# Optimization experiments

Measured on AMD Instinct MI355X. Metric: run time of the kernel, lower is better.

Reference implementation:

```python
import jax, jax.numpy as jnp
import numpy as np

H = 1024      # hidden_size
V = 32000     # output_size (vocab)
L = 128       # max_length (encoder length)
B = 256       # batch


def setup_inputs() -> dict:
    key = jax.random.key(0)
    ks = jax.random.split(key, 16)
    s = 1.0 / np.sqrt(H)
    inp = {
        "input_ids": jax.random.randint(ks[0], (1, B), 0, V),
        "hidden": jax.random.normal(ks[1], (1, B, H), dtype=jnp.float32),
        "encoder_outputs": jax.random.normal(ks[2], (B, L, H), dtype=jnp.float32),
        # parameters
        "emb_table": jax.random.normal(ks[3], (V, H), dtype=jnp.float32),
        "attn_w": jax.random.uniform(ks[4], (L, 2 * H), jnp.float32, -s, s),
        "attn_b": jax.random.uniform(ks[5], (L,), jnp.float32, -s, s),
        "comb_w": jax.random.uniform(ks[6], (H, 2 * H), jnp.float32, -s, s),
        "comb_b": jax.random.uniform(ks[7], (H,), jnp.float32, -s, s),
        "w_ih": jax.random.uniform(ks[8], (3 * H, H), jnp.float32, -s, s),
        "b_ih": jax.random.uniform(ks[9], (3 * H,), jnp.float32, -s, s),
        "w_hh": jax.random.uniform(ks[10], (3 * H, H), jnp.float32, -s, s),
        "b_hh": jax.random.uniform(ks[11], (3 * H,), jnp.float32, -s, s),
        "out_w": jax.random.uniform(ks[12], (V, H), jnp.float32, -s, s),
        "out_b": jax.random.uniform(ks[13], (V,), jnp.float32, -s, s),
    }
    return inp


def reference(input_ids, hidden, encoder_outputs, emb_table,
              attn_w, attn_b, comb_w, comb_b,
              w_ih, b_ih, w_hh, b_hh, out_w, out_b):
    # embedding: input_ids (1, B) -> embedded (1, B, H); dropout is identity in eval
    embedded = emb_table[input_ids]            # (1, B, H)
    emb0 = embedded[0]                         # (B, H)
    h0 = hidden[0]                             # (B, H)

    # Bahdanau-style attention over fixed encoder length L
    attn_logits = jnp.concatenate([emb0, h0], axis=1) @ attn_w.T + attn_b   # (B, L)
    attn_weights = jax.nn.softmax(attn_logits, axis=1)                      # (B, L)
    attn_applied = jnp.einsum("bl,blh->bh", attn_weights, encoder_outputs)  # (B, H)

    # combine + relu
    x = jnp.concatenate([emb0, attn_applied], axis=1) @ comb_w.T + comb_b   # (B, H)
    x = jax.nn.relu(x)

    # single GRU step (PyTorch gate layout: r, z, n)
    gx = x @ w_ih.T + b_ih                     # (B, 3H)
    gh = h0 @ w_hh.T + b_hh                    # (B, 3H)
    xr, xz, xn = jnp.split(gx, 3, axis=1)
    hr, hz, hn = jnp.split(gh, 3, axis=1)
    r = jax.nn.sigmoid(xr + hr)
    z = jax.nn.sigmoid(xz + hz)
    n = jnp.tanh(xn + r * hn)
    h_new = (1.0 - z) * n + z * h0             # (B, H)

    logp = jax.nn.log_softmax(h_new @ out_w.T + out_b, axis=1)   # (B, V)
    return logp, h_new[None], attn_weights
```

## Files before the change

kernel.cpp:

```cpp
#include <hip/hip_runtime.h>
#include <hip/hip_bf16.h>
#include <math.h>

#define H 1024
#define L 128
#define B 256
#define V 32000

typedef __attribute__((ext_vector_type(8))) short bf16x8;
typedef __attribute__((ext_vector_type(4))) float f32x4;

static __device__ __forceinline__ ushort f2bf(float f) {
    unsigned int u = __float_as_uint(f);
    u += 0x7fffu + ((u >> 16) & 1u);
    return (ushort)(u >> 16);
}

__global__ __launch_bounds__(256) void attn_kernel(
    const int* __restrict__ input_ids,
    const float* __restrict__ hidden,
    const float* __restrict__ enc,
    const float* __restrict__ emb_table,
    const float* __restrict__ attn_w,
    const float* __restrict__ attn_b,
    ushort* __restrict__ xcat_b16,
    ushort* __restrict__ h0_b16,
    float* __restrict__ attn_weights_out)
{
    __shared__ float s_e[H];
    __shared__ float s_h[H];
    __shared__ float s_part[256];
    __shared__ float s_w[L];
    __shared__ float s_wr[4];

    const int b = blockIdx.x;
    const int tid = threadIdx.x;

    const int id = input_ids[b];
    const float4* e4 = (const float4*)(emb_table + (size_t)id * H);
    const float4* h4 = (const float4*)(hidden + (size_t)b * H);

    float4 ev = e4[tid];
    float4 hv = h4[tid];
    ((float4*)s_e)[tid] = ev;
    ((float4*)s_h)[tid] = hv;

    {
        uint2 p;
        p.x = (unsigned)f2bf(ev.x) | ((unsigned)f2bf(ev.y) << 16);
        p.y = (unsigned)f2bf(ev.z) | ((unsigned)f2bf(ev.w) << 16);
        *(uint2*)(xcat_b16 + (size_t)b * 2 * H + tid * 4) = p;
        uint2 q;
        q.x = (unsigned)f2bf(hv.x) | ((unsigned)f2bf(hv.y) << 16);
        q.y = (unsigned)f2bf(hv.z) | ((unsigned)f2bf(hv.w) << 16);
        *(uint2*)(h0_b16 + (size_t)b * H + tid * 4) = q;
    }
    __syncthreads();

    const int l = tid & 127;
    const int half = tid >> 7;
    const float4* w4 = (const float4*)(attn_w + (size_t)l * (2 * H) + half * H);
    const float4* s4 = (const float4*)(half ? s_h : s_e);
    float acc = 0.f;
#pragma unroll 4
    for (int k = 0; k < H / 4; ++k) {
        float4 w = w4[k];
        float4 s = s4[k];
        acc += w.x * s.x + w.y * s.y + w.z * s.z + w.w * s.w;
    }
    s_part[tid] = acc;
    __syncthreads();
    if (tid < L) s_w[tid] = s_part[tid] + s_part[tid + 128] + attn_b[tid];
    __syncthreads();

    const int wid = tid >> 6;
    float v = (tid < L) ? s_w[tid] : -INFINITY;
    for (int off = 32; off; off >>= 1) v = fmaxf(v, __shfl_xor(v, off));
    if ((tid & 63) == 0) s_wr[wid] = v;
    __syncthreads();
    const float m = fmaxf(s_wr[0], s_wr[1]);

    float e = 0.f;
    if (tid < L) e = __expf(s_w[tid] - m);
    float sv = e;
    for (int off = 32; off; off >>= 1) sv += __shfl_xor(sv, off);
    __syncthreads();
    if ((tid & 63) == 0) s_wr[wid] = sv;
    __syncthreads();
    const float inv = 1.f / (s_wr[0] + s_wr[1]);
    if (tid < L) {
        float w = e * inv;
        s_w[tid] = w;
        attn_weights_out[(size_t)b * L + tid] = w;
    }
    __syncthreads();

    const float4* enc4 = (const float4*)(enc + (size_t)b * L * H);
    float4 a = {0.f, 0.f, 0.f, 0.f};
#pragma unroll 4
    for (int ll = 0; ll < L; ++ll) {
        const float w = s_w[ll];
        float4 e2 = enc4[(size_t)ll * (H / 4) + tid];
        a.x += w * e2.x; a.y += w * e2.y; a.z += w * e2.z; a.w += w * e2.w;
    }
    {
        uint2 p;
        p.x = (unsigned)f2bf(a.x) | ((unsigned)f2bf(a.y) << 16);
        p.y = (unsigned)f2bf(a.z) | ((unsigned)f2bf(a.w) << 16);
        *(uint2*)(xcat_b16 + (size_t)b * 2 * H + H + tid * 4) = p;
    }
}

template<int K, int MODE>
__global__ __launch_bounds__(256) void mfma_gemm(
    const ushort* __restrict__ A,
    const float* __restrict__ W,
    const float* __restrict__ bias,
    float* __restrict__ outf,
    ushort* __restrict__ outb,
    float* __restrict__ rowsum,
    int N)
{
    constexpr int NT = 32;
    __shared__ ushort sA[256 * 72];
    __shared__ ushort sW[NT * 72];
    __shared__ float sLse[256];

    const int tid = threadIdx.x;
    const int bn = blockIdx.x * NT;
    const int w = tid >> 6;
    const int l = tid & 63;
    const int g = l >> 4;
    const int ln = l & 15;
    const int trow = tid >> 3;
    const int tcol = tid & 7;

    if (MODE == 3) sLse[tid] = __logf(rowsum[tid]);

    f32x4 acc[4][2];
#pragma unroll
    for (int i = 0; i < 4; ++i)
#pragma unroll
        for (int n = 0; n < 2; ++n)
            acc[i][n] = (f32x4){0.f, 0.f, 0.f, 0.f};

    for (int k0 = 0; k0 < K; k0 += 64) {
#pragma unroll
        for (int p = 0; p < 8; ++p) {
            const int r = p * 32 + trow;
            uint4 v = *(const uint4*)(A + (size_t)r * K + k0 + tcol * 8);
            *(uint4*)(sA + r * 72 + tcol * 8) = v;
        }
        {
            const float* wp = W + (size_t)(bn + trow) * K + k0 + tcol * 8;
            float4 w0 = *(const float4*)(wp);
            float4 w1 = *(const float4*)(wp + 4);
            ushort tmp[8];
            tmp[0] = f2bf(w0.x); tmp[1] = f2bf(w0.y); tmp[2] = f2bf(w0.z); tmp[3] = f2bf(w0.w);
            tmp[4] = f2bf(w1.x); tmp[5] = f2bf(w1.y); tmp[6] = f2bf(w1.z); tmp[7] = f2bf(w1.w);
            *(uint4*)(sW + trow * 72 + tcol * 8) = *(const uint4*)tmp;
        }
        __syncthreads();
#pragma unroll
        for (int s = 0; s < 2; ++s) {
            bf16x8 af[4], bfr[2];
#pragma unroll
            for (int i = 0; i < 4; ++i)
                af[i] = *(const bf16x8*)(sA + (64 * w + 16 * i + ln) * 72 + s * 32 + g * 8);
#pragma unroll
            for (int n = 0; n < 2; ++n)
                bfr[n] = *(const bf16x8*)(sW + (16 * n + ln) * 72 + s * 32 + g * 8);
#pragma unroll
            for (int i = 0; i < 4; ++i)
#pragma unroll
                for (int n = 0; n < 2; ++n)
                    acc[i][n] = __builtin_amdgcn_mfma_f32_16x16x32_bf16(af[i], bfr[n], acc[i][n], 0, 0, 0);
        }
        __syncthreads();
    }

    const float b0 = bias[bn + ln];
    const float b1 = bias[bn + 16 + ln];

    if (MODE == 0) {
#pragma unroll
        for (int i = 0; i < 4; ++i)
#pragma unroll
            for (int n = 0; n < 2; ++n)
#pragma unroll
                for (int r = 0; r < 4; ++r)
                    outf[(size_t)(64 * w + 16 * i + 4 * g + r) * N + bn + 16 * n + ln] =
                        acc[i][n][r] + (n ? b1 : b0);
    } else if (MODE == 1) {
#pragma unroll
        for (int i = 0; i < 4; ++i)
#pragma unroll
            for (int n = 0; n < 2; ++n)
#pragma unroll
                for (int r = 0; r < 4; ++r) {
                    float vv = acc[i][n][r] + (n ? b1 : b0);
                    vv = fmaxf(vv, 0.f);
                    outb[(size_t)(64 * w + 16 * i + 4 * g + r) * N + bn + 16 * n + ln] = f2bf(vv);
                }
    } else if (MODE == 2) {
#pragma unroll
        for (int i = 0; i < 4; ++i) {
            float e[4];
#pragma unroll
            for (int r = 0; r < 4; ++r)
                e[r] = __expf(acc[i][0][r] + b0) + __expf(acc[i][1][r] + b1);
#pragma unroll
            for (int msk = 1; msk < 16; msk <<= 1)
#pragma unroll
                for (int r = 0; r < 4; ++r)
                    e[r] += __shfl_xor(e[r], msk);
            if (ln < 4)
                atomicAdd(&rowsum[64 * w + 16 * i + 4 * g + ln], e[ln]);
        }
    } else {
#pragma unroll
        for (int i = 0; i < 4; ++i)
#pragma unroll
            for (int n = 0; n < 2; ++n)
#pragma unroll
                for (int r = 0; r < 4; ++r) {
                    const int row = 64 * w + 16 * i + 4 * g + r;
                    outf[(size_t)row * N + bn + 16 * n + ln] =
                        acc[i][n][r] + (n ? b1 : b0) - sLse[row];
                }
    }
}

__global__ __launch_bounds__(256) void gru_kernel(
    const float* __restrict__ gx,
    const float* __restrict__ gh,
    const float* __restrict__ h0,
    float* __restrict__ h_new,
    ushort* __restrict__ hn_b16,
    float* __restrict__ rowsum)
{
    if (blockIdx.x == 0) rowsum[threadIdx.x] = 0.f;
    const int idx = blockIdx.x * 256 + threadIdx.x;
    const int b = idx >> 10;
    const int j = idx & (H - 1);
    const size_t base = (size_t)b * 3 * H;
    const float xr = gx[base + j];
    const float xz = gx[base + H + j];
    const float xn = gx[base + 2 * H + j];
    const float hr = gh[base + j];
    const float hz = gh[base + H + j];
    const float hn = gh[base + 2 * H + j];
    const float r = 1.f / (1.f + __expf(-(xr + hr)));
    const float z = 1.f / (1.f + __expf(-(xz + hz)));
    const float n = tanhf(xn + r * hn);
    const float out = (1.f - z) * n + z * h0[idx];
    h_new[idx] = out;
    hn_b16[idx] = f2bf(out);
}

extern "C" void kernel_launch(void* const* d_in, const int* in_sizes, int n_in,
                              void* d_out, int out_size, void* d_ws, size_t ws_size,
                              hipStream_t stream) {
    const int*   input_ids = (const int*)d_in[0];
    const float* hidden    = (const float*)d_in[1];
    const float* enc       = (const float*)d_in[2];
    const float* emb_table = (const float*)d_in[3];
    const float* attn_w    = (const float*)d_in[4];
    const float* attn_b    = (const float*)d_in[5];
    const float* comb_w    = (const float*)d_in[6];
    const float* comb_b    = (const float*)d_in[7];
    const float* w_ih      = (const float*)d_in[8];
    const float* b_ih      = (const float*)d_in[9];
    const float* w_hh      = (const float*)d_in[10];
    const float* b_hh      = (const float*)d_in[11];
    const float* out_w     = (const float*)d_in[12];
    const float* out_b     = (const float*)d_in[13];

    float* out = (float*)d_out;
    float* logp         = out;
    float* h_new        = out + (size_t)B * V;
    float* attn_weights = h_new + (size_t)B * H;

    ushort* xcat_b16 = (ushort*)d_ws;
    ushort* h0_b16   = xcat_b16 + (size_t)B * 2 * H;
    ushort* x_b16    = h0_b16 + (size_t)B * H;
    ushort* hn_b16   = x_b16 + (size_t)B * H;
    float*  gx       = (float*)(hn_b16 + (size_t)B * H);
    float*  gh       = gx + (size_t)B * 3 * H;
    float*  rowsum   = gh + (size_t)B * 3 * H;

    attn_kernel<<<dim3(B), dim3(256), 0, stream>>>(
        input_ids, hidden, enc, emb_table, attn_w, attn_b,
        xcat_b16, h0_b16, attn_weights);

    mfma_gemm<2 * H, 1><<<dim3(H / 32), dim3(256), 0, stream>>>(
        xcat_b16, comb_w, comb_b, nullptr, x_b16, nullptr, H);

    mfma_gemm<H, 0><<<dim3(3 * H / 32), dim3(256), 0, stream>>>(
        x_b16, w_ih, b_ih, gx, nullptr, nullptr, 3 * H);

    mfma_gemm<H, 0><<<dim3(3 * H / 32), dim3(256), 0, stream>>>(
        h0_b16, w_hh, b_hh, gh, nullptr, nullptr, 3 * H);

    gru_kernel<<<dim3(B * H / 256), dim3(256), 0, stream>>>(
        gx, gh, hidden, h_new, hn_b16, rowsum);

    mfma_gemm<H, 2><<<dim3(V / 32), dim3(256), 0, stream>>>(
        hn_b16, out_w, out_b, nullptr, nullptr, rowsum, V);

    mfma_gemm<H, 3><<<dim3(V / 32), dim3(256), 0, stream>>>(
        hn_b16, out_w, out_b, logp, nullptr, rowsum, V);
}
```

Before: 589.2 us.

## Split attention apply across blocks, add M-tiling and register prefetch to GEMMs

Attention is split in two kernels. One computes the softmax weights. The other applies them to the encoder outputs over an (8, B) grid, so each batch row's 512KB read is spread across more blocks. The generic GEMM gains template parameters for block size and M/N tile sizes plus a 2D grid, so the small GEMMs launch many more blocks. It also prefetches the next K-slice into registers while MFMA runs on the current one. The vocab GEMMs now use 512-thread blocks with 64-wide N tiles, which halves W re-reads per block but raises register pressure.

```diff
diff --git a/kernel.cpp b/kernel.cpp
--- a/kernel.cpp
+++ b/kernel.cpp
@@ -16,10 +16,9 @@
     return (ushort)(u >> 16);
 }
 
-__global__ __launch_bounds__(256) void attn_kernel(
+__global__ __launch_bounds__(256) void attn_softmax_kernel(
     const int* __restrict__ input_ids,
     const float* __restrict__ hidden,
-    const float* __restrict__ enc,
     const float* __restrict__ emb_table,
     const float* __restrict__ attn_w,
     const float* __restrict__ attn_b,
@@ -37,11 +36,8 @@
     const int tid = threadIdx.x;
 
     const int id = input_ids[b];
-    const float4* e4 = (const float4*)(emb_table + (size_t)id * H);
-    const float4* h4 = (const float4*)(hidden + (size_t)b * H);
-
-    float4 ev = e4[tid];
-    float4 hv = h4[tid];
+    float4 ev = ((const float4*)(emb_table + (size_t)id * H))[tid];
+    float4 hv = ((const float4*)(hidden + (size_t)b * H))[tid];
     ((float4*)s_e)[tid] = ev;
     ((float4*)s_h)[tid] = hv;
 
@@ -88,31 +84,53 @@
     if ((tid & 63) == 0) s_wr[wid] = sv;
     __syncthreads();
     const float inv = 1.f / (s_wr[0] + s_wr[1]);
-    if (tid < L) {
-        float w = e * inv;
-        s_w[tid] = w;
-        attn_weights_out[(size_t)b * L + tid] = w;
-    }
-    __syncthreads();
-
-    const float4* enc4 = (const float4*)(enc + (size_t)b * L * H);
+    if (tid < L) attn_weights_out[(size_t)b * L + tid] = e * inv;
+}
+
+__global__ __launch_bounds__(256) void attn_apply_kernel(
+    const float* __restrict__ enc,
+    const float* __restrict__ attn_weights,
+    ushort* __restrict__ xcat_b16)
+{
+    __shared__ float s_w[L];
+    __shared__ float4 s_red[256];
+
+    const int c = blockIdx.x;
+    const int b = blockIdx.y;
+    const int tid = threadIdx.x;
+    const int lg = tid >> 5;
+    const int hc = tid & 31;
+
+    if (tid < L) s_w[tid] = attn_weights[(size_t)b * L + tid];
+    __syncthreads();
+
+    const float4* enc4 = (const float4*)enc;
     float4 a = {0.f, 0.f, 0.f, 0.f};
-#pragma unroll 4
-    for (int ll = 0; ll < L; ++ll) {
+#pragma unroll
+    for (int it = 0; it < 16; ++it) {
+        const int ll = it * 8 + lg;
         const float w = s_w[ll];
-        float4 e2 = enc4[(size_t)ll * (H / 4) + tid];
+        float4 e2 = enc4[((size_t)b * L + ll) * (H / 4) + c * 32 + hc];
         a.x += w * e2.x; a.y += w * e2.y; a.z += w * e2.z; a.w += w * e2.w;
     }
-    {
+    s_red[tid] = a;
+    __syncthreads();
+    if (tid < 32) {
+        float4 t = s_red[tid];
+#pragma unroll
+        for (int j = 1; j < 8; ++j) {
+            float4 o = s_red[j * 32 + tid];
+            t.x += o.x; t.y += o.y; t.z += o.z; t.w += o.w;
+        }
         uint2 p;
-        p.x = (unsigned)f2bf(a.x) | ((unsigned)f2bf(a.y) << 16);
-        p.y = (unsigned)f2bf(a.z) | ((unsigned)f2bf(a.w) << 16);
-        *(uint2*)(xcat_b16 + (size_t)b * 2 * H + H + tid * 4) = p;
-    }
-}
-
-template<int K, int MODE>
-__global__ __launch_bounds__(256) void mfma_gemm(
+        p.x = (unsigned)f2bf(t.x) | ((unsigned)f2bf(t.y) << 16);
+        p.y = (unsigned)f2bf(t.z) | ((unsigned)f2bf(t.w) << 16);
+        *(uint2*)(xcat_b16 + (size_t)b * 2 * H + H + c * 128 + tid * 4) = p;
+    }
+}
+
+template<int BLK, int MT, int NT, int K, int MODE>
+__global__ __launch_bounds__(BLK) void mfma_gemm(
     const ushort* __restrict__ A,
     const float* __restrict__ W,
     const float* __restrict__ bias,
@@ -121,112 +139,151 @@
     float* __restrict__ rowsum,
     int N)
 {
-    constexpr int NT = 32;
-    __shared__ ushort sA[256 * 72];
-    __shared__ ushort sW[NT * 72];
-    __shared__ float sLse[256];
+    constexpr int WAVES = BLK / 64;
+    constexpr int RPW = MT / WAVES;
+    constexpr int NI = RPW / 16;
+    constexpr int NN = NT / 16;
+    constexpr int PA = (MT * 8) / BLK;
+    constexpr int PW = (NT * 8 + BLK - 1) / BLK;
+    constexpr int LDA = 72;
+
+    __shared__ ushort sA[MT * LDA];
+    __shared__ ushort sW[NT * LDA];
+    __shared__ float sLse[MT];
 
     const int tid = threadIdx.x;
     const int bn = blockIdx.x * NT;
-    const int w = tid >> 6;
-    const int l = tid & 63;
-    const int g = l >> 4;
-    const int ln = l & 15;
+    const int bm = blockIdx.y * MT;
+    const int wv = tid >> 6;
+    const int lane = tid & 63;
+    const int g = lane >> 4;
+    const int ln = lane & 15;
     const int trow = tid >> 3;
     const int tcol = tid & 7;
 
-    if (MODE == 3) sLse[tid] = __logf(rowsum[tid]);
-
-    f32x4 acc[4][2];
-#pragma unroll
-    for (int i = 0; i < 4; ++i)
-#pragma unroll
-        for (int n = 0; n < 2; ++n)
+    if (MODE == 3 && tid < MT) sLse[tid] = __logf(rowsum[bm + tid]);
+
+    uint4 aReg[PA];
+    float4 wReg[PW][2];
+
+    auto prefetch = [&](int k0) {
+#pragma unroll
+        for (int p = 0; p < PA; ++p) {
+            const int r = p * (BLK / 8) + trow;
+            aReg[p] = *(const uint4*)(A + (size_t)(bm + r) * K + k0 + tcol * 8);
+        }
+#pragma unroll
+        for (int p = 0; p < PW; ++p) {
+            const int r = p * (BLK / 8) + trow;
+            if (NT * 8 >= BLK || r < NT) {
+                const float* wp = W + (size_t)(bn + r) * K + k0 + tcol * 8;
+                wReg[p][0] = *(const float4*)wp;
+                wReg[p][1] = *(const float4*)(wp + 4);
+            }
+        }
+    };
+    auto stage = [&]() {
+#pragma unroll
+        for (int p = 0; p < PA; ++p) {
+            const int r = p * (BLK / 8) + trow;
+            *(uint4*)(sA + r * LDA + tcol * 8) = aReg[p];
+        }
+#pragma unroll
+        for (int p = 0; p < PW; ++p) {
+            const int r = p * (BLK / 8) + trow;
+            if (NT * 8 >= BLK || r < NT) {
+                ushort t[8];
+                t[0] = f2bf(wReg[p][0].x); t[1] = f2bf(wReg[p][0].y);
+                t[2] = f2bf(wReg[p][0].z); t[3] = f2bf(wReg[p][0].w);
+                t[4] = f2bf(wReg[p][1].x); t[5] = f2bf(wReg[p][1].y);
+                t[6] = f2bf(wReg[p][1].z); t[7] = f2bf(wReg[p][1].w);
+                *(uint4*)(sW + r * LDA + tcol * 8) = *(const uint4*)t;
+            }
+        }
+    };
+
+    f32x4 acc[NI][NN];
+#pragma unroll
+    for (int i = 0; i < NI; ++i)
+#pragma unroll
+        for (int n = 0; n < NN; ++n)
             acc[i][n] = (f32x4){0.f, 0.f, 0.f, 0.f};
 
+    prefetch(0);
     for (int k0 = 0; k0 < K; k0 += 64) {
-#pragma unroll
-        for (int p = 0; p < 8; ++p) {
-            const int r = p * 32 + trow;
-            uint4 v = *(const uint4*)(A + (size_t)r * K + k0 + tcol * 8);
-            *(uint4*)(sA + r * 72 + tcol * 8) = v;
-        }
-        {
-            const float* wp = W + (size_t)(bn + trow) * K + k0 + tcol * 8;
-            float4 w0 = *(const float4*)(wp);
-            float4 w1 = *(const float4*)(wp + 4);
-            ushort tmp[8];
-            tmp[0] = f2bf(w0.x); tmp[1] = f2bf(w0.y); tmp[2] = f2bf(w0.z); tmp[3] = f2bf(w0.w);
-            tmp[4] = f2bf(w1.x); tmp[5] = f2bf(w1.y); tmp[6] = f2bf(w1.z); tmp[7] = f2bf(w1.w);
-            *(uint4*)(sW + trow * 72 + tcol * 8) = *(const uint4*)tmp;
-        }
         __syncthreads();
+        stage();
+        __syncthreads();
+        if (k0 + 64 < K) prefetch(k0 + 64);
 #pragma unroll
         for (int s = 0; s < 2; ++s) {
-            bf16x8 af[4], bfr[2];
-#pragma unroll
-            for (int i = 0; i < 4; ++i)
-                af[i] = *(const bf16x8*)(sA + (64 * w + 16 * i + ln) * 72 + s * 32 + g * 8);
-#pragma unroll
-            for (int n = 0; n < 2; ++n)
-                bfr[n] = *(const bf16x8*)(sW + (16 * n + ln) * 72 + s * 32 + g * 8);
-#pragma unroll
-            for (int i = 0; i < 4; ++i)
-#pragma unroll
-                for (int n = 0; n < 2; ++n)
+            bf16x8 af[NI], bfr[NN];
+#pragma unroll
+            for (int i = 0; i < NI; ++i)
+                af[i] = *(const bf16x8*)(sA + (wv * RPW + 16 * i + ln) * LDA + s * 32 + g * 8);
+#pragma unroll
+            for (int n = 0; n < NN; ++n)
+                bfr[n] = *(const bf16x8*)(sW + (16 * n + ln) * LDA + s * 32 + g * 8);
+#pragma unroll
+            for (int i = 0; i < NI; ++i)
+#pragma unroll
+                for (int n = 0; n < NN; ++n)
                     acc[i][n] = __builtin_amdgcn_mfma_f32_16x16x32_bf16(af[i], bfr[n], acc[i][n], 0, 0, 0);
         }
-        __syncthreads();
-    }
-
-    const float b0 = bias[bn + ln];
-    const float b1 = bias[bn + 16 + ln];
+    }
+
+    float bb[NN];
+#pragma unroll
+    for (int n = 0; n < NN; ++n) bb[n] = bias[bn + 16 * n + ln];
 
     if (MODE == 0) {
 #pragma unroll
-        for (int i = 0; i < 4; ++i)
-#pragma unroll
-            for (int n = 0; n < 2; ++n)
+        for (int i = 0; i < NI; ++i)
+#pragma unroll
+            for (int n = 0; n < NN; ++n)
 #pragma unroll
                 for (int r = 0; r < 4; ++r)
-                    outf[(size_t)(64 * w + 16 * i + 4 * g + r) * N + bn + 16 * n + ln] =
-                        acc[i][n][r] + (n ? b1 : b0);
+                    outf[(size_t)(bm + wv * RPW + 16 * i + 4 * g + r) * N + bn + 16 * n + ln] =
+                        acc[i][n][r] + bb[n];
     } else if (MODE == 1) {
 #pragma unroll
-        for (int i = 0; i < 4; ++i)
-#pragma unroll
-            for (int n = 0; n < 2; ++n)
+        for (int i = 0; i < NI; ++i)
+#pragma unroll
+            for (int n = 0; n < NN; ++n)
 #pragma unroll
                 for (int r = 0; r < 4; ++r) {
-                    float vv = acc[i][n][r] + (n ? b1 : b0);
-                    vv = fmaxf(vv, 0.f);
-                    outb[(size_t)(64 * w + 16 * i + 4 * g + r) * N + bn + 16 * n + ln] = f2bf(vv);
+                    float vv = fmaxf(acc[i][n][r] + bb[n], 0.f);
+                    outb[(size_t)(bm + wv * RPW + 16 * i + 4 * g + r) * N + bn + 16 * n + ln] = f2bf(vv);
                 }
     } else if (MODE == 2) {
 #pragma unroll
-        for (int i = 0; i < 4; ++i) {
+        for (int i = 0; i < NI; ++i) {
             float e[4];
 #pragma unroll
-            for (int r = 0; r < 4; ++r)
-                e[r] = __expf(acc[i][0][r] + b0) + __expf(acc[i][1][r] + b1);
+            for (int r = 0; r < 4; ++r) {
+                e[r] = 0.f;
+#pragma unroll
+                for (int n = 0; n < NN; ++n)
+                    e[r] += __expf(acc[i][n][r] + bb[n]);
+            }
 #pragma unroll
             for (int msk = 1; msk < 16; msk <<= 1)
 #pragma unroll
                 for (int r = 0; r < 4; ++r)
                     e[r] += __shfl_xor(e[r], msk);
             if (ln < 4)
-                atomicAdd(&rowsum[64 * w + 16 * i + 4 * g + ln], e[ln]);
+                atomicAdd(&rowsum[bm + wv * RPW + 16 * i + 4 * g + ln], e[ln]);
         }
     } else {
 #pragma unroll
-        for (int i = 0; i < 4; ++i)
-#pragma unroll
-            for (int n = 0; n < 2; ++n)
+        for (int i = 0; i < NI; ++i)
+#pragma unroll
+            for (int n = 0; n < NN; ++n)
 #pragma unroll
                 for (int r = 0; r < 4; ++r) {
-                    const int row = 64 * w + 16 * i + 4 * g + r;
-                    outf[(size_t)row * N + bn + 16 * n + ln] =
-                        acc[i][n][r] + (n ? b1 : b0) - sLse[row];
+                    const int lrow = wv * RPW + 16 * i + 4 * g + r;
+                    outf[(size_t)(bm + lrow) * N + bn + 16 * n + ln] =
+                        acc[i][n][r] + bb[n] - sLse[lrow];
                 }
     }
 }
@@ -289,25 +346,28 @@
     float*  gh       = gx + (size_t)B * 3 * H;
     float*  rowsum   = gh + (size_t)B * 3 * H;
 
-    attn_kernel<<<dim3(B), dim3(256), 0, stream>>>(
-        input_ids, hidden, enc, emb_table, attn_w, attn_b,
+    attn_softmax_kernel<<<dim3(B), dim3(256), 0, stream>>>(
+        input_ids, hidden, emb_table, attn_w, attn_b,
         xcat_b16, h0_b16, attn_weights);
 
-    mfma_gemm<2 * H, 1><<<dim3(H / 32), dim3(256), 0, stream>>>(
+    attn_apply_kernel<<<dim3(8, B), dim3(256), 0, stream>>>(
+        enc, attn_weights, xcat_b16);
+
+    mfma_gemm<256, 64, 16, 2 * H, 1><<<dim3(H / 16, B / 64), dim3(256), 0, stream>>>(
         xcat_b16, comb_w, comb_b, nullptr, x_b16, nullptr, H);
 
-    mfma_gemm<H, 0><<<dim3(3 * H / 32), dim3(256), 0, stream>>>(
+    mfma_gemm<256, 64, 32, H, 0><<<dim3(3 * H / 32, B / 64), dim3(256), 0, stream>>>(
         x_b16, w_ih, b_ih, gx, nullptr, nullptr, 3 * H);
 
-    mfma_gemm<H, 0><<<dim3(3 * H / 32), dim3(256), 0, stream>>>(
+    mfma_gemm<256, 64, 32, H, 0><<<dim3(3 * H / 32, B / 64), dim3(256), 0, stream>>>(
         h0_b16, w_hh, b_hh, gh, nullptr, nullptr, 3 * H);
 
     gru_kernel<<<dim3(B * H / 256), dim3(256), 0, stream>>>(
         gx, gh, hidden, h_new, hn_b16, rowsum);
 
-    mfma_gemm<H, 2><<<dim3(V / 32), dim3(256), 0, stream>>>(
+    mfma_gemm<512, 256, 64, H, 2><<<dim3(V / 64, 1), dim3(512), 0, stream>>>(
         hn_b16, out_w, out_b, nullptr, nullptr, rowsum, V);
 
-    mfma_gemm<H, 3><<<dim3(V / 32), dim3(256), 0, stream>>>(
+    mfma_gemm<512, 256, 64, H, 3><<<dim3(V / 64, 1), dim3(512), 0, stream>>>(
         hn_b16, out_w, out_b, logp, nullptr, rowsum, V);
 }
```

Result: slower. 637.0 us (+8.1%).
